# Optimization experiments

Measured on AMD Instinct MI355X. Metric: run time of the kernel, lower is better.

The kernel has to match this reference:

```python
import jax, jax.numpy as jnp
import numpy as np

B, L = 1024, 64          # sentences, tokens per sentence
V, E = 100000, 300       # vocab, embedding dim
RH, M, NC = 50, 50, 3    # rnn_hidden, mem_dim, num_class
N = B * L                # total tree nodes


def setup_inputs() -> dict:
    key = jax.random.key(0)
    ks = jax.random.split(key, 24)
    rn = lambda k, s, sc=0.05: jax.random.normal(k, s, dtype=jnp.float32) * sc
    # balanced binary dependency tree per sentence: parent(i) = (i-1)//2
    loc = np.arange(L)
    par_loc = np.where(loc == 0, -1, (loc - 1) // 2)
    parent = np.where(par_loc[None, :] < 0, -1,
                      par_loc[None, :] + np.arange(B)[:, None] * L).reshape(-1)
    depth = np.tile(np.floor(np.log2(loc + 1)).astype(np.int64), B)
    tm = np.zeros(L, np.float32); tm[1:4] = 1.0  # 3 aspect-target tokens/sentence
    return {
        "embed_ids": jax.random.randint(ks[0], (B, L), 0, V),
        "parent": jnp.asarray(parent),
        "depth": jnp.asarray(depth),
        "target_mask": jnp.asarray(np.tile(tm, B)),
        "num_levels": 7,
        "embed_table": rn(ks[1], (V, E), 1.0),
        "W_ih_f": rn(ks[2], (4 * RH, E)), "W_hh_f": rn(ks[3], (4 * RH, RH)),
        "b_f": rn(ks[4], (4 * RH,)),
        "W_ih_b": rn(ks[5], (4 * RH, E)), "W_hh_b": rn(ks[6], (4 * RH, RH)),
        "b_b": rn(ks[7], (4 * RH,)),
        "W_iou": rn(ks[8], (3 * M, 2 * RH)),
        "U_iou_w": rn(ks[9], (3 * M, M)), "U_iou_b": rn(ks[10], (3 * M,)),
        "b_iou": jnp.zeros((3 * M,), jnp.float32),
        "U_f_w": rn(ks[11], (M, M)), "U_f_b": rn(ks[12], (M,)),
        "H_w": rn(ks[13], (M, 2 * RH)), "H_b": rn(ks[14], (M,)),
        "C_w": rn(ks[15], (NC, M)), "C_b": rn(ks[16], (NC,)),
    }


def _lstm(x, W_ih, W_hh, b, reverse):
    # x: (B, L, E) -> (B, L, H); PyTorch gate order i, f, g, o
    xg = jnp.einsum('ble,ge->blg', x, W_ih) + b
    H = W_hh.shape[1]
    def step(carry, xt):
        h, c = carry
        g = xt + h @ W_hh.T
        i, f, gg, o = jnp.split(g, 4, axis=-1)
        c = jax.nn.sigmoid(f) * c + jax.nn.sigmoid(i) * jnp.tanh(gg)
        h = jax.nn.sigmoid(o) * jnp.tanh(c)
        return (h, c), h
    z = jnp.zeros((x.shape[0], H), x.dtype)
    _, hs = jax.lax.scan(step, (z, z), jnp.swapaxes(xg, 0, 1), reverse=reverse)
    return jnp.swapaxes(hs, 0, 1)


def reference(embed_ids, parent, depth, target_mask, num_levels, embed_table,
              W_ih_f, W_hh_f, b_f, W_ih_b, W_hh_b, b_b,
              W_iou, U_iou_w, U_iou_b, b_iou, U_f_w, U_f_b,
              H_w, H_b, C_w, C_b):
    # --- BiLSTM encoder (dropout = identity at inference) ---
    emb = embed_table[embed_ids]                       # (B,L,E) gather
    hf = _lstm(emb, W_ih_f, W_hh_f, b_f, False)
    hb = _lstm(emb, W_ih_b, W_hh_b, b_b, True)
    x = jnp.concatenate([hf, hb], -1).reshape(N, 2 * RH)
    # --- ChildSum TreeLSTM, topological (deepest level first) ---
    iou0 = x @ W_iou.T                                 # (N, 3M)
    h_init = x @ H_w.T + H_b                           # (N, M)
    parent_safe = jnp.where(parent >= 0, parent, N)    # roots -> dummy slot N
    counts = jnp.zeros(N + 1, jnp.int32).at[parent_safe].add(1)
    has_children = (counts[:N] > 0)[:, None]
    h_fin = h_init
    c_fin = jnp.zeros((N, M), jnp.float32)
    h_sum = jnp.zeros((N + 1, M), jnp.float32)         # sum of child h
    fc_sum = jnp.zeros((N + 1, M), jnp.float32)        # sum of f * child c
    for lvl in range(num_levels - 1, -1, -1):
        m = (depth == lvl)[:, None]
        # reduce: leaves never get U_iou bias (no mailbox in DGL)
        iou = iou0 + jnp.where(has_children, h_sum[:N] @ U_iou_w.T + U_iou_b, 0.0) + b_iou
        i, o, u = jnp.split(iou, 3, axis=-1)
        c_new = jax.nn.sigmoid(i) * jnp.tanh(u) + fc_sum[:N]
        h_new = h_init + jax.nn.sigmoid(o) * jnp.tanh(c_new)
        h_fin = jnp.where(m, h_new, h_fin)
        c_fin = jnp.where(m, c_new, c_fin)
        # scatter messages from this level's nodes to their parents
        f = jax.nn.sigmoid(h_new @ U_f_w.T + U_f_b)
        h_sum = h_sum.at[parent_safe].add(jnp.where(m, h_new, 0.0))
        fc_sum = fc_sum.at[parent_safe].add(jnp.where(m, f * c_new, 0.0))
    # --- masked mean pool over target tokens per sentence ---
    tm = target_mask.reshape(B, L)
    pooled = (h_fin.reshape(B, L, M) * tm[:, :, None]).sum(1) / tm.sum(1, keepdims=True)
    logits = pooled @ C_w.T + C_b
    return logits, pooled
```

## Files before the change

kernel.cpp:

```cpp
#include <hip/hip_runtime.h>


typedef __attribute__((ext_vector_type(8))) short bf16x8;
typedef __attribute__((ext_vector_type(4))) float f32x4;

__device__ __forceinline__ float fsig(float x) { return 1.0f / (1.0f + __expf(-x)); }
__device__ __forceinline__ float ftanh(float x) {
    float a = fabsf(x);
    float t = __expf(2.0f * a);
    float r = 1.0f - 2.0f / (t + 1.0f);
    return copysignf(r, x);
}
__device__ __forceinline__ float fsig2(float x) {
    float e = __builtin_amdgcn_exp2f(-1.4426950408889634f * x);
    return __builtin_amdgcn_rcpf(1.0f + e);
}
__device__ __forceinline__ float ftanh2(float x) {
    float e = __builtin_amdgcn_exp2f(2.8853900817779268f * x);
    return 1.0f - 2.0f * __builtin_amdgcn_rcpf(1.0f + e);
}

__device__ __forceinline__ unsigned short rne_bf16(float f) {
    unsigned u = __builtin_bit_cast(unsigned, f);
    unsigned r = u + 0x7fffu + ((u >> 16) & 1u);
    return (unsigned short)(r >> 16);
}
__device__ __forceinline__ void split2(float f, unsigned short& h, unsigned short& l) {
    h = rne_bf16(f);
    float fh = __builtin_bit_cast(float, ((unsigned)h) << 16);
    float r = f - fh;
    l = rne_bf16(r);
}

__device__ __forceinline__ void async_lds16(const void* g, void* l) {
    __builtin_amdgcn_global_load_lds(
        (const __attribute__((address_space(1))) unsigned int*)g,
        (__attribute__((address_space(3))) unsigned int*)l, 16, 0, 0);
}

__device__ __forceinline__ bf16x8 pack8(const unsigned short* h) {
    bf16x8 v;
    #pragma unroll
    for (int e = 0; e < 8; ++e) v[e] = (short)h[e];
    return v;
}

__global__ void conv_kernel(const float* __restrict__ B1, const float* __restrict__ B2,
                            int split, int K, int Rreal, int BN, int KCH,
                            unsigned short* __restrict__ out) {
    int q = blockIdx.x * 256 + threadIdx.x;
    int total = KCH * 4 * BN;
    if (q >= total) return;
    int n  = q % BN;
    int kq = (q / BN) & 3;
    int c  = q / (BN * 4);
    const float* row = (n < split) ? (B1 + (size_t)n * K) : (B2 + (size_t)(n - split) * K);
    unsigned short h[8], l[8];
    #pragma unroll
    for (int e = 0; e < 8; ++e) {
        int k = c * 32 + kq * 8 + e;
        float v = (n < Rreal && k < K) ? row[k] : 0.0f;
        split2(v, h[e], l[e]);
    }
    size_t hb = ((((size_t)c * 2 + 0) * 4 + kq) * BN + n) * 8;
    size_t lb = ((((size_t)c * 2 + 1) * 4 + kq) * BN + n) * 8;
    *(ushort4*)&out[hb]     = make_ushort4(h[0], h[1], h[2], h[3]);
    *(ushort4*)&out[hb + 4] = make_ushort4(h[4], h[5], h[6], h[7]);
    *(ushort4*)&out[lb]     = make_ushort4(l[0], l[1], l[2], l[3]);
    *(ushort4*)&out[lb + 4] = make_ushort4(l[4], l[5], l[6], l[7]);
}

template<int BN, int KCH, int KREAL, int NCOLS, bool GATHER>
__global__ __launch_bounds__(256)
void gemm_split(const float* __restrict__ A, const int* __restrict__ ids,
                const unsigned short* __restrict__ Bc,
                const float* __restrict__ bias1, const float* __restrict__ bias2,
                int split, float* __restrict__ C) {
    constexpr int NTW = BN / 64;
    __shared__ __align__(16) unsigned short As[2 * 4 * 64 * 8];
    __shared__ __align__(16) unsigned short Bt[64 * BN];

    const int tid = threadIdx.x;
    const int m0 = blockIdx.x * 64;
    const int w = tid >> 6, lane = tid & 63;
    const int r16 = lane & 15, quad = lane >> 4;
    const int wn = w * (BN / 4);

    const int mA = tid & 63, kqA = tid >> 6;
    const float* arow = GATHER ? (A + (size_t)ids[m0 + mA] * KREAL)
                               : (A + (size_t)(m0 + mA) * KREAL);

    float ar[8];
    {
        int k0 = kqA * 8;
        if (k0 + 8 <= KREAL) {
            float4 p = *(const float4*)(arow + k0);
            float4 q = *(const float4*)(arow + k0 + 4);
            ar[0]=p.x; ar[1]=p.y; ar[2]=p.z; ar[3]=p.w;
            ar[4]=q.x; ar[5]=q.y; ar[6]=q.z; ar[7]=q.w;
        } else {
            #pragma unroll
            for (int e = 0; e < 8; ++e) ar[e] = (k0 + e < KREAL) ? arow[k0 + e] : 0.0f;
        }
    }

    f32x4 acc[4][NTW] = {};

    for (int c = 0; c < KCH; ++c) {
        __syncthreads();
        {
            const unsigned short* src = Bc + (size_t)c * 64 * BN + tid * 8;
            #pragma unroll
            for (int i = 0; i < BN / 32; ++i)
                async_lds16(src + (size_t)i * 2048, Bt + i * 2048 + tid * 8);
        }
        {
            unsigned short h[8], l[8];
            #pragma unroll
            for (int e = 0; e < 8; ++e) split2(ar[e], h[e], l[e]);
            *(bf16x8*)&As[((0 * 4 + kqA) * 64 + mA) * 8] = pack8(h);
            *(bf16x8*)&As[((1 * 4 + kqA) * 64 + mA) * 8] = pack8(l);
        }
        __syncthreads();
        if (c + 1 < KCH) {
            int k0 = (c + 1) * 32 + kqA * 8;
            if (k0 + 8 <= KREAL) {
                float4 p = *(const float4*)(arow + k0);
                float4 q = *(const float4*)(arow + k0 + 4);
                ar[0]=p.x; ar[1]=p.y; ar[2]=p.z; ar[3]=p.w;
                ar[4]=q.x; ar[5]=q.y; ar[6]=q.z; ar[7]=q.w;
            } else {
                #pragma unroll
                for (int e = 0; e < 8; ++e) ar[e] = (k0 + e < KREAL) ? arow[k0 + e] : 0.0f;
            }
        }
        bf16x8 af[2][4];
        #pragma unroll
        for (int i = 0; i < 4; ++i) {
            af[0][i] = *(const bf16x8*)&As[((0 * 4 + quad) * 64 + i * 16 + r16) * 8];
            af[1][i] = *(const bf16x8*)&As[((1 * 4 + quad) * 64 + i * 16 + r16) * 8];
        }
        #pragma unroll
        for (int t = 0; t < NTW; ++t) {
            bf16x8 bh = *(const bf16x8*)&Bt[((0 * 4 + quad) * BN + wn + t * 16 + r16) * 8];
            bf16x8 bl = *(const bf16x8*)&Bt[((1 * 4 + quad) * BN + wn + t * 16 + r16) * 8];
            #pragma unroll
            for (int i = 0; i < 4; ++i) {
                acc[i][t] = __builtin_amdgcn_mfma_f32_16x16x32_bf16(af[0][i], bh, acc[i][t], 0, 0, 0);
                acc[i][t] = __builtin_amdgcn_mfma_f32_16x16x32_bf16(af[1][i], bh, acc[i][t], 0, 0, 0);
                acc[i][t] = __builtin_amdgcn_mfma_f32_16x16x32_bf16(af[0][i], bl, acc[i][t], 0, 0, 0);
            }
        }
    }

    #pragma unroll
    for (int t = 0; t < NTW; ++t) {
        int ncol = wn + t * 16 + r16;
        if (ncol < NCOLS) {
            float bv = (ncol < split) ? bias1[ncol] : bias2[ncol - split];
            #pragma unroll
            for (int i = 0; i < 4; ++i)
                #pragma unroll
                for (int r = 0; r < 4; ++r) {
                    int mrow = m0 + i * 16 + quad * 4 + r;
                    C[(size_t)mrow * NCOLS + ncol] = acc[i][t][r] + bv;
                }
        }
    }
}

constexpr int WHC_DIR = 2 * 2 * 4 * 208 * 8;

__global__ __launch_bounds__(256)
void lstm_mfma(const float* __restrict__ xg, const unsigned short* __restrict__ Whc,
               float* __restrict__ x) {
    const int bi = blockIdx.x;
    const int dir = bi & 1;
    const int b0 = (bi >> 1) * 16;
    const int tid = threadIdx.x;
    const int w = tid >> 6, lane = tid & 63;
    const int r16 = lane & 15, quad = lane >> 4;

    __shared__ __align__(16) unsigned short Ah[8 * 16 * 8];
    __shared__ __align__(16) unsigned short Al[8 * 16 * 8];
    __shared__ __align__(16) float G[208 * 20];
    __shared__ __align__(16) float Xs[2][16][268];

    const int n0 = (w == 0) ? 0 : (w == 1) ? 4 : (w == 2) ? 7 : 10;
    const int nc = (w == 0) ? 4 : 3;

    const unsigned short* Wd = Whc + (size_t)dir * WHC_DIR;
    bf16x8 bfr[4][2][2];
    #pragma unroll
    for (int t = 0; t < 4; ++t) {
        int col = (n0 + ((t < nc) ? t : 0)) * 16 + r16;
        #pragma unroll
        for (int c = 0; c < 2; ++c)
            #pragma unroll
            for (int h = 0; h < 2; ++h)
                bfr[t][c][h] = *(const bf16x8*)&Wd[((((size_t)c * 2 + h) * 4 + quad) * 208 + col) * 8];
    }

    for (int q = tid; q < 512; q += 256) {
        ((unsigned*)Ah)[q] = 0u;
        ((unsigned*)Al)[q] = 0u;
    }

    int ss[4], ms[4];
    #pragma unroll
    for (int j = 0; j < 4; ++j) {
        int q = tid + 256 * j;
        ss[j] = q & 15;
        ms[j] = q >> 4;
    }
    float c_reg[4] = {0.0f, 0.0f, 0.0f, 0.0f};

    {
        int idx0 = dir ? 63 : 0;
        #pragma unroll
        for (int i = 0; i < 4; ++i) {
            int s = w * 4 + i;
            const float* src = xg + ((size_t)(b0 + s) * 64 + idx0) * 400 + dir * 200 + lane * 4;
            async_lds16(src, &Xs[0][s][lane * 4]);
        }
    }
    __syncthreads();

    for (int step = 0; step < 64; ++step) {
        const int buf = step & 1;
        const int idx = dir ? (63 - step) : step;
        if (step < 63) {
            const int idxn = dir ? (62 - step) : (step + 1);
            #pragma unroll
            for (int i = 0; i < 4; ++i) {
                int s = w * 4 + i;
                const float* src = xg + ((size_t)(b0 + s) * 64 + idxn) * 400 + dir * 200 + lane * 4;
                async_lds16(src, &Xs[buf ^ 1][s][lane * 4]);
            }
        }
        bf16x8 ah[2], al[2];
        #pragma unroll
        for (int c = 0; c < 2; ++c) {
            ah[c] = *(const bf16x8*)&Ah[((c * 4 + quad) * 16 + r16) * 8];
            al[c] = *(const bf16x8*)&Al[((c * 4 + quad) * 16 + r16) * 8];
        }
        f32x4 acc[4] = {};
        #pragma unroll
        for (int t = 0; t < 4; ++t) {
            if (t < nc) {
                #pragma unroll
                for (int c = 0; c < 2; ++c) {
                    acc[t] = __builtin_amdgcn_mfma_f32_16x16x32_bf16(ah[c], bfr[t][c][0], acc[t], 0, 0, 0);
                    acc[t] = __builtin_amdgcn_mfma_f32_16x16x32_bf16(al[c], bfr[t][c][0], acc[t], 0, 0, 0);
                    acc[t] = __builtin_amdgcn_mfma_f32_16x16x32_bf16(ah[c], bfr[t][c][1], acc[t], 0, 0, 0);
                }
            }
        }
        #pragma unroll
        for (int t = 0; t < 4; ++t) {
            if (t < nc) {
                int col = (n0 + t) * 16 + r16;
                *(f32x4*)&G[col * 20 + quad * 4] = acc[t];
            }
        }
        __syncthreads();
        #pragma unroll
        for (int j = 0; j < 4; ++j) {
            if (tid + 256 * j < 800) {
                int s = ss[j], m = ms[j];
                float gi = G[m * 20 + s]         + Xs[buf][s][m];
                float gf = G[(m + 50) * 20 + s]  + Xs[buf][s][m + 50];
                float gg = G[(m + 100) * 20 + s] + Xs[buf][s][m + 100];
                float go = G[(m + 150) * 20 + s] + Xs[buf][s][m + 150];
                c_reg[j] = fsig2(gf) * c_reg[j] + fsig2(gi) * ftanh2(gg);
                float h = fsig2(go) * ftanh2(c_reg[j]);
                unsigned short hh, hl;
                split2(h, hh, hl);
                Ah[(m >> 3) * 128 + s * 8 + (m & 7)] = hh;
                Al[(m >> 3) * 128 + s * 8 + (m & 7)] = hl;
                x[((size_t)(b0 + s) * 64 + idx) * 100 + dir * 50 + m] = h;
            }
        }
        __syncthreads();
    }
}

__global__ __launch_bounds__(256)
void tree_kernel(const float* __restrict__ C2,
                 const float* __restrict__ Uw, const float* __restrict__ Ub,
                 const float* __restrict__ Fw, const float* __restrict__ Fb,
                 const float* __restrict__ tmask,
                 const float* __restrict__ Cw, const float* __restrict__ Cb,
                 float* __restrict__ out) {
    const int b = blockIdx.x;
    const int tid = threadIdx.x;

    __shared__ __align__(16) float h_sum[32][52];
    __shared__ __align__(16) float fc_sum[32][52];
    __shared__ __align__(16) float hcur[32][52];
    __shared__ __align__(16) float mcur[32][52];
    __shared__ float msg[16][152];
    __shared__ float hfin[64][50];
    __shared__ float pool[52];

    const int rU = (tid < 150) ? tid : 0;
    const int rF = tid % 50;
    float ur[50], fr[50];
    #pragma unroll
    for (int k = 0; k < 50; ++k) ur[k] = Uw[rU * 50 + k];
    #pragma unroll
    for (int k = 0; k < 50; ++k) fr[k] = Fw[rF * 50 + k];
    const float ub = Ub[rU];
    const float fb = Fb[rF];

    for (int q = tid; q < 32 * 52; q += 256) {
        h_sum[q / 52][q % 52] = 0.0f;
        fc_sum[q / 52][q % 52] = 0.0f;
    }
    __syncthreads();

    const float* c2b = C2 + (size_t)b * 64 * 200;

    for (int lvl = 6; lvl >= 0; --lvl) {
        const int lo = (1 << lvl) - 1;
        const int hi = min((1 << (lvl + 1)) - 2, 63);
        const int A = hi - lo + 1;
        const int chn = max(0, min(hi, 31) - lo + 1);

        if (tid < 150) {
            for (int a = 0; a < chn; ++a) {
                float acc = ub;
                #pragma unroll
                for (int k4 = 0; k4 < 12; ++k4) {
                    float4 h4 = *(const float4*)&h_sum[lo + a][k4 * 4];
                    acc += ur[k4*4+0]*h4.x + ur[k4*4+1]*h4.y + ur[k4*4+2]*h4.z + ur[k4*4+3]*h4.w;
                }
                acc += ur[48]*h_sum[lo + a][48] + ur[49]*h_sum[lo + a][49];
                msg[a][tid] = acc;
            }
        }
        __syncthreads();

        for (int q = tid; q < A * 50; q += 256) {
            int a = q / 50, m = q - a * 50;
            int loc = lo + a;
            const float* base = c2b + (size_t)loc * 200;
            bool ch = (a < chn);
            float ig = base[m]       + (ch ? msg[a][m]       : 0.0f);
            float og = base[50 + m]  + (ch ? msg[a][50 + m]  : 0.0f);
            float ug = base[100 + m] + (ch ? msg[a][100 + m] : 0.0f);
            float cn = fsig(ig) * ftanh(ug) + (ch ? fc_sum[loc][m] : 0.0f);
            float hn = base[150 + m] + fsig(og) * ftanh(cn);
            hcur[a][m] = hn;
            mcur[a][m] = cn;
            hfin[loc][m] = hn;
        }
        __syncthreads();

        if (tid < 250) {
            for (int a = tid / 50; a < A; a += 5) {
                float acc = fb;
                #pragma unroll
                for (int k4 = 0; k4 < 12; ++k4) {
                    float4 h4 = *(const float4*)&hcur[a][k4 * 4];
                    acc += fr[k4*4+0]*h4.x + fr[k4*4+1]*h4.y + fr[k4*4+2]*h4.z + fr[k4*4+3]*h4.w;
                }
                acc += fr[48]*hcur[a][48] + fr[49]*hcur[a][49];
                mcur[a][rF] = fsig(acc) * mcur[a][rF];
            }
        }
        __syncthreads();

        if (lvl > 0) {
            const int plo = (lo - 1) >> 1, phi = (hi - 1) >> 1;
            const int P = phi - plo + 1;
            for (int q = tid; q < P * 50; q += 256) {
                int pi = q / 50, m = q - pi * 50;
                int p = plo + pi;
                int c1 = 2 * p + 1, c2i = 2 * p + 2;
                float hs = hcur[c1 - lo][m];
                float fs = mcur[c1 - lo][m];
                if (c2i <= hi) { hs += hcur[c2i - lo][m]; fs += mcur[c2i - lo][m]; }
                h_sum[p][m] += hs;
                fc_sum[p][m] += fs;
            }
        }
        __syncthreads();
    }

    const float* tm = tmask + (size_t)b * 64;
    if (tid < 50) {
        float acc = 0.0f, ws = 0.0f;
        for (int l = 0; l < 64; ++l) {
            float wv = tm[l];
            ws += wv;
            acc += wv * hfin[l][tid];
        }
        float p = acc / ws;
        pool[tid] = p;
        out[3072 + (size_t)b * 50 + tid] = p;
    }
    __syncthreads();
    if (tid < 3) {
        float acc = Cb[tid];
        #pragma unroll
        for (int m = 0; m < 50; ++m) acc += Cw[tid * 50 + m] * pool[m];
        out[(size_t)b * 3 + tid] = acc;
    }
}

extern "C" void kernel_launch(void* const* d_in, const int* in_sizes, int n_in,
                              void* d_out, int out_size, void* d_ws, size_t ws_size,
                              hipStream_t stream) {
    (void)in_sizes; (void)n_in; (void)out_size; (void)ws_size;
    const int*   ids   = (const int*)d_in[0];
    const float* tmask = (const float*)d_in[3];
    const float* table = (const float*)d_in[5];
    const float* Wihf  = (const float*)d_in[6];
    const float* Whhf  = (const float*)d_in[7];
    const float* bf    = (const float*)d_in[8];
    const float* Wihb  = (const float*)d_in[9];
    const float* Whhb  = (const float*)d_in[10];
    const float* bb    = (const float*)d_in[11];
    const float* Wiou  = (const float*)d_in[12];
    const float* Uiouw = (const float*)d_in[13];
    const float* Uioub = (const float*)d_in[14];
    const float* biou  = (const float*)d_in[15];
    const float* Ufw   = (const float*)d_in[16];
    const float* Ufb   = (const float*)d_in[17];
    const float* Hw    = (const float*)d_in[18];
    const float* Hb    = (const float*)d_in[19];
    const float* Cw    = (const float*)d_in[20];
    const float* Cb    = (const float*)d_in[21];
    float* out = (float*)d_out;

    float* wsf = (float*)d_ws;
    float* xg = wsf;
    float* x  = wsf + (size_t)65536 * 400;
    float* C2 = wsf;
    unsigned short* B1c = (unsigned short*)(wsf + 32768000);
    unsigned short* B3c = (unsigned short*)(wsf + 32911360);
    unsigned short* Whc = (unsigned short*)(wsf + 32944128);

    conv_kernel<<<70, 256, 0, stream>>>(Wihf, Wihb, 200, 300, 400, 448, 10, B1c);
    conv_kernel<<<16, 256, 0, stream>>>(Wiou, Hw, 150, 100, 200, 256, 4, B3c);
    conv_kernel<<<7, 256, 0, stream>>>(Whhf, Whhf, 200, 50, 200, 208, 2, Whc);
    conv_kernel<<<7, 256, 0, stream>>>(Whhb, Whhb, 200, 50, 200, 208, 2, Whc + WHC_DIR);
    gemm_split<448, 10, 300, 400, true><<<1024, 256, 0, stream>>>(
        table, ids, B1c, bf, bb, 200, xg);
    lstm_mfma<<<128, 256, 0, stream>>>(xg, Whc, x);
    gemm_split<256, 4, 100, 200, false><<<1024, 256, 0, stream>>>(
        x, nullptr, B3c, biou, Hb, 150, C2);
    tree_kernel<<<1024, 256, 0, stream>>>(
        C2, Uiouw, Uioub, Ufw, Ufb, tmask, Cw, Cb, out);
}
```

Measured before the change: 455.4 us.

## Prefetch LSTM input gates into registers two steps ahead, drop LDS staging

Replaces the double-buffered async global-to-LDS staging of the precomputed input gates with per-thread register loads issued two timesteps ahead, unrolling the recurrence by two so the buffers alternate. It also swaps __syncthreads for a barrier that waits only on lgkmcnt, so outstanding global loads do not stall the barrier. This removes LDS traffic and the vmcnt wait from each step of the serial recurrence. In exchange it uses scattered, less-coalesced global loads (stride 50 per gate) and more registers. Correctness now depends on the vector loads finishing before use through compiler-inserted waits.

```diff
diff --git a/kernel.cpp b/kernel.cpp
--- a/kernel.cpp
+++ b/kernel.cpp
@@ -184,7 +184,6 @@
     __shared__ __align__(16) unsigned short Ah[8 * 16 * 8];
     __shared__ __align__(16) unsigned short Al[8 * 16 * 8];
     __shared__ __align__(16) float G[208 * 20];
-    __shared__ __align__(16) float Xs[2][16][268];
 
     const int n0 = (w == 0) ? 0 : (w == 1) ? 4 : (w == 2) ? 7 : 10;
     const int nc = (w == 0) ? 4 : 3;
@@ -207,37 +206,33 @@
     }
 
     int ss[4], ms[4];
+    bool act[4];
     #pragma unroll
     for (int j = 0; j < 4; ++j) {
         int q = tid + 256 * j;
         ss[j] = q & 15;
         ms[j] = q >> 4;
+        act[j] = (q < 800);
     }
     float c_reg[4] = {0.0f, 0.0f, 0.0f, 0.0f};
 
-    {
-        int idx0 = dir ? 63 : 0;
-        #pragma unroll
-        for (int i = 0; i < 4; ++i) {
-            int s = w * 4 + i;
-            const float* src = xg + ((size_t)(b0 + s) * 64 + idx0) * 400 + dir * 200 + lane * 4;
-            async_lds16(src, &Xs[0][s][lane * 4]);
-        }
-    }
-    __syncthreads();
-
-    for (int step = 0; step < 64; ++step) {
-        const int buf = step & 1;
+    auto issue = [&](int step, float (&xr)[4][4]) {
         const int idx = dir ? (63 - step) : step;
-        if (step < 63) {
-            const int idxn = dir ? (62 - step) : (step + 1);
-            #pragma unroll
-            for (int i = 0; i < 4; ++i) {
-                int s = w * 4 + i;
-                const float* src = xg + ((size_t)(b0 + s) * 64 + idxn) * 400 + dir * 200 + lane * 4;
-                async_lds16(src, &Xs[buf ^ 1][s][lane * 4]);
-            }
-        }
+        const float* base = xg + (size_t)b0 * 25600 + (size_t)idx * 400 + dir * 200;
+        #pragma unroll
+        for (int j = 0; j < 4; ++j) {
+            if (act[j]) {
+                const float* p = base + (size_t)ss[j] * 25600 + ms[j];
+                xr[j][0] = p[0];
+                xr[j][1] = p[50];
+                xr[j][2] = p[100];
+                xr[j][3] = p[150];
+            }
+        }
+    };
+
+    auto do_step = [&](int step, float (&xcur)[4][4]) {
+        const int idx = dir ? (63 - step) : step;
         bf16x8 ah[2], al[2];
         #pragma unroll
         for (int c = 0; c < 2; ++c) {
@@ -263,15 +258,15 @@
                 *(f32x4*)&G[col * 20 + quad * 4] = acc[t];
             }
         }
-        __syncthreads();
+        asm volatile("s_waitcnt lgkmcnt(0)\n\ts_barrier" ::: "memory");
         #pragma unroll
         for (int j = 0; j < 4; ++j) {
-            if (tid + 256 * j < 800) {
+            if (act[j]) {
                 int s = ss[j], m = ms[j];
-                float gi = G[m * 20 + s]         + Xs[buf][s][m];
-                float gf = G[(m + 50) * 20 + s]  + Xs[buf][s][m + 50];
-                float gg = G[(m + 100) * 20 + s] + Xs[buf][s][m + 100];
-                float go = G[(m + 150) * 20 + s] + Xs[buf][s][m + 150];
+                float gi = G[m * 20 + s]         + xcur[j][0];
+                float gf = G[(m + 50) * 20 + s]  + xcur[j][1];
+                float gg = G[(m + 100) * 20 + s] + xcur[j][2];
+                float go = G[(m + 150) * 20 + s] + xcur[j][3];
                 c_reg[j] = fsig2(gf) * c_reg[j] + fsig2(gi) * ftanh2(gg);
                 float h = fsig2(go) * ftanh2(c_reg[j]);
                 unsigned short hh, hl;
@@ -281,7 +276,18 @@
                 x[((size_t)(b0 + s) * 64 + idx) * 100 + dir * 50 + m] = h;
             }
         }
-        __syncthreads();
+        if (step < 62) issue(step + 2, xcur);
+        asm volatile("s_waitcnt lgkmcnt(0)\n\ts_barrier" ::: "memory");
+    };
+
+    float xr0[4][4], xr1[4][4];
+    issue(0, xr0);
+    issue(1, xr1);
+    __syncthreads();
+
+    for (int s2 = 0; s2 < 32; ++s2) {
+        do_step(2 * s2,     xr0);
+        do_step(2 * s2 + 1, xr1);
     }
 }
 
```

Result: slower. 524.9 us (+15.2%).
